# Kernel optimization log

Hardware: AMD Instinct MI355X
Metric: run time of the kernel (lower is better)

## Reference

```python
import jax, jax.numpy as jnp
import numpy as np

D_MODEL = 4096
N_Q_HEAD = 32
N_KV_HEAD = 8
HEAD_DIM = D_MODEL // N_Q_HEAD  # 128
N_REP = N_Q_HEAD // N_KV_HEAD   # 4
B, T = 2, 2048


def _rope_tables(seq_len, head_dim, dtype=jnp.float32):
    # theta_i = 10000^(-2*(i-1)/d) for i=1..d/2  (matches torch.pow(10000, -2*(arange(1,d/2+1)-1)/d))
    i = jnp.arange(head_dim // 2, dtype=dtype)
    theta = jnp.power(10000.0, -2.0 * i / head_dim)
    angles = jnp.outer(jnp.arange(seq_len, dtype=dtype), theta)  # [T, d/2]
    return jnp.cos(angles), jnp.sin(angles)


def _apply_rope(x, cos, sin):
    # x: [B, T, h, HD]; pairs are consecutive elements (view_as_complex semantics)
    B_, T_, h, hd = x.shape
    xp = x.reshape(B_, T_, h, hd // 2, 2)
    xr, xi = xp[..., 0], xp[..., 1]
    c = cos[None, :T_, None, :]
    s = sin[None, :T_, None, :]
    out_r = xr * c - xi * s
    out_i = xr * s + xi * c
    return jnp.stack([out_r, out_i], axis=-1).reshape(B_, T_, h, hd)


def setup_inputs() -> dict:
    key = jax.random.key(0)
    ks = jax.random.split(key, 5)
    scale = 0.02
    x = jax.random.normal(ks[0], (B, T, D_MODEL), dtype=jnp.float32)
    wq = jax.random.normal(ks[1], (D_MODEL, N_Q_HEAD * HEAD_DIM), dtype=jnp.float32) * scale
    wk = jax.random.normal(ks[2], (D_MODEL, N_KV_HEAD * HEAD_DIM), dtype=jnp.float32) * scale
    wv = jax.random.normal(ks[3], (D_MODEL, N_KV_HEAD * HEAD_DIM), dtype=jnp.float32) * scale
    wo = jax.random.normal(ks[4], (N_Q_HEAD * HEAD_DIM, D_MODEL), dtype=jnp.float32) * scale
    # causal mask: 1 where masked (strict upper triangle), per masked_fill(mask==1, -inf)
    attention_mask = jnp.triu(jnp.ones((T, T), dtype=jnp.int32), k=1)
    return {"x": x, "wq": wq, "wk": wk, "wv": wv, "wo": wo, "attention_mask": attention_mask}


def reference(x, wq, wk, wv, wo, attention_mask):
    B_, T_, _ = x.shape
    xq = (x @ wq).reshape(B_, T_, N_Q_HEAD, HEAD_DIM)
    xk = (x @ wk).reshape(B_, T_, N_KV_HEAD, HEAD_DIM)
    xv = (x @ wv).reshape(B_, T_, N_KV_HEAD, HEAD_DIM)

    cos, sin = _rope_tables(T_, HEAD_DIM, x.dtype)
    xq = _apply_rope(xq, cos, sin)
    xk = _apply_rope(xk, cos, sin)

    # GQA: repeat kv heads (training path: no cache)
    xk = jnp.repeat(xk, N_REP, axis=2)  # [B, T, HQ, HD]
    xv = jnp.repeat(xv, N_REP, axis=2)

    q = xq.transpose(0, 2, 1, 3)  # [B, H, T, HD]
    k = xk.transpose(0, 2, 1, 3)
    v = xv.transpose(0, 2, 1, 3)

    scores = jnp.einsum('bhqd,bhkd->bhqk', q, k) / jnp.sqrt(jnp.asarray(HEAD_DIM, x.dtype))
    scores = jnp.where(attention_mask[None, None, :, :] == 1, -jnp.inf, scores)
    probs = jax.nn.softmax(scores, axis=-1)
    out = jnp.einsum('bhqk,bhkd->bhqd', probs, v)
    out = out.transpose(0, 2, 1, 3).reshape(B_, T_, N_Q_HEAD * HEAD_DIM)
    return out @ wo
```

## Files before the change

kernel.cpp:

```cpp
#include <hip/hip_runtime.h>
#include <hip/hip_bf16.h>
#include <math.h>

typedef __hip_bfloat16 bf16;
typedef short bf16x8 __attribute__((ext_vector_type(8)));
typedef float f32x4 __attribute__((ext_vector_type(4)));
typedef float f32x16 __attribute__((ext_vector_type(16)));
typedef unsigned int u32;
typedef unsigned short u16;

#define GLD16(g, l)                                                            \
  __builtin_amdgcn_global_load_lds(                                            \
      (const __attribute__((address_space(1))) void*)(g),                      \
      (__attribute__((address_space(3))) void*)(l), 16, 0, 0)

#define SBAR() __builtin_amdgcn_s_barrier()
#define VMCNT(n) asm volatile("s_waitcnt vmcnt(" #n ")")
#define LGKM0() asm volatile("s_waitcnt lgkmcnt(0)")

__global__ void convert_f32_bf16(const float* __restrict__ in,
                                 bf16* __restrict__ out) {
  size_t i = ((size_t)blockIdx.x * 256 + threadIdx.x) * 4;
  float4 v = *(const float4*)(in + i);
  out[i + 0] = __float2bfloat16(v.x);
  out[i + 1] = __float2bfloat16(v.y);
  out[i + 2] = __float2bfloat16(v.z);
  out[i + 3] = __float2bfloat16(v.w);
}

__global__ void transpose_f32_bf16(const float* __restrict__ in,
                                   bf16* __restrict__ out, int R, int C) {
  __shared__ bf16 tile[32][33];
  int tx = threadIdx.x & 31, ty = threadIdx.x >> 5;
  int c0 = blockIdx.x * 32, r0 = blockIdx.y * 32;
#pragma unroll
  for (int i = 0; i < 32; i += 8)
    tile[ty + i][tx] = __float2bfloat16(in[(size_t)(r0 + ty + i) * C + c0 + tx]);
  __syncthreads();
#pragma unroll
  for (int i = 0; i < 32; i += 8)
    out[(size_t)(c0 + ty + i) * R + r0 + tx] = tile[tx][ty + i];
}

__global__ void transpose_v(const bf16* __restrict__ V, bf16* __restrict__ VT) {
  __shared__ bf16 tile[32][33];
  int s = blockIdx.z, b = s >> 3, kvh = s & 7;
  int t0 = blockIdx.x * 32, d0 = blockIdx.y * 32;
  int tx = threadIdx.x & 31, ty = threadIdx.x >> 5;
#pragma unroll
  for (int i = 0; i < 32; i += 8)
    tile[ty + i][tx] =
        V[(size_t)(b * 2048 + t0 + ty + i) * 6144 + kvh * 128 + d0 + tx];
  __syncthreads();
#pragma unroll
  for (int i = 0; i < 32; i += 8)
    VT[((size_t)s * 128 + d0 + ty + i) * 2048 + t0 + tx] = tile[tx][ty + i];
}

__global__ void rope_table_k(float* __restrict__ tab) {
  int idx = blockIdx.x * 256 + threadIdx.x;
  int t = idx >> 6, i = idx & 63;
  float theta = powf(10000.0f, -2.0f * (float)i / 128.0f);
  float ang = (float)t * theta;
  tab[idx * 2 + 0] = cosf(ang);
  tab[idx * 2 + 1] = sinf(ang);
}

__global__ void rope_apply(bf16* __restrict__ X, const float* __restrict__ tab,
                           int nheads, int rowstride, float omul) {
  size_t idx = (size_t)blockIdx.x * 256 + threadIdx.x;
  int i = (int)(idx & 63);
  size_t rest = idx >> 6;
  int h = (int)(rest % nheads);
  size_t r = rest / nheads;
  int t = (int)(r & 2047);
  float c = tab[(t * 64 + i) * 2 + 0];
  float s = tab[(t * 64 + i) * 2 + 1];
  bf16* p = X + r * (size_t)rowstride + h * 128 + 2 * i;
  float xr = __bfloat162float(p[0]), xi = __bfloat162float(p[1]);
  p[0] = __float2bfloat16((xr * c - xi * s) * omul);
  p[1] = __float2bfloat16((xr * s + xi * c) * omul);
}

template <typename OutT>
__global__ __launch_bounds__(512, 2) void gemm_bt8(const bf16* __restrict__ A,
                                                   const bf16* __restrict__ BT,
                                                   OutT* __restrict__ C, int M,
                                                   int N, int K) {
  __shared__ bf16 AS[2][2][128 * 64];
  __shared__ bf16 BS[2][2][128 * 64];

  const int tid = threadIdx.x;
  const int lane = tid & 63;
  const int w = tid >> 6, wm = w >> 2, wn = w & 3;
  const int lr = lane & 15, hi = lane >> 4;

  int gx = gridDim.x;
  int nwg = gx * gridDim.y;
  int bid = blockIdx.y * gx + blockIdx.x;
  int swz = (bid & 7) * (nwg >> 3) + (bid >> 3);
  const int m0 = (swz / gx) * 256, n0 = (swz % gx) * 256;

  const int NKT = K >> 6;
  const int NI = K >> 7;
  const int srow = tid >> 3;
  const int scol = ((tid & 7) ^ (srow & 7)) << 3;

  f32x4 acc[8][4];
#pragma unroll
  for (int m = 0; m < 8; ++m)
#pragma unroll
    for (int n = 0; n < 4; ++n)
#pragma unroll
      for (int j = 0; j < 4; ++j) acc[m][n][j] = 0.f;

  auto STAGE_A = [&](int buf, int kt) {
    int kk0 = (kt < NKT) ? kt * 64 : 0;
#pragma unroll
    for (int hs = 0; hs < 4; ++hs) {
      int ha = hs >> 1, sa = hs & 1;
      const bf16* g = A + (size_t)(m0 + ha * 128 + sa * 64 + srow) * K + kk0 + scol;
      GLD16(g, &AS[buf][ha][(sa * 64 + srow) * 64 + (tid & 7) * 8]);
    }
  };
  auto STAGE_B = [&](int buf, int kt, int half) {
    int kk0 = (kt < NKT) ? kt * 64 : 0;
#pragma unroll
    for (int sa = 0; sa < 2; ++sa) {
      const bf16* g =
          BT + (size_t)(n0 + half * 128 + sa * 64 + srow) * K + kk0 + scol;
      GLD16(g, &BS[buf][half][(sa * 64 + srow) * 64 + (tid & 7) * 8]);
    }
  };

  bf16x8 bfr[4][2], af[2][2];
  auto READ_B = [&](int buf) {
#pragma unroll
    for (int n = 0; n < 4; ++n) {
      int row = (wn & 1) * 64 + n * 16 + lr;
#pragma unroll
      for (int kk = 0; kk < 2; ++kk)
        bfr[n][kk] = *(const bf16x8*)(&BS[buf][wn >> 1]
                                         [row * 64 + (((kk * 4 + hi) ^ (row & 7)) << 3)]);
    }
  };
  auto READ_A = [&](int buf, int q) {
#pragma unroll
    for (int mm = 0; mm < 2; ++mm) {
      int row = (q * 2 + mm) * 16 + lr;
#pragma unroll
      for (int kk = 0; kk < 2; ++kk)
        af[mm][kk] = *(const bf16x8*)(&AS[buf][wm]
                                         [row * 64 + (((kk * 4 + hi) ^ (row & 7)) << 3)]);
    }
  };

#define MFMA16(q)                                                              \
  do {                                                                         \
    LGKM0();                                                                   \
    __builtin_amdgcn_s_setprio(1);                                             \
    _Pragma("unroll") for (int mm = 0; mm < 2; ++mm)                           \
        _Pragma("unroll") for (int n = 0; n < 4; ++n)                          \
        _Pragma("unroll") for (int kk = 0; kk < 2; ++kk)                       \
            acc[(q) * 2 + mm][n] = __builtin_amdgcn_mfma_f32_16x16x32_bf16(    \
                af[mm][kk], bfr[n][kk], acc[(q) * 2 + mm][n], 0, 0, 0);        \
    __builtin_amdgcn_s_setprio(0);                                             \
  } while (0)

  STAGE_A(0, 0);
  STAGE_B(0, 0, 0);
  STAGE_B(0, 0, 1);
  STAGE_B(1, 1, 0);
  STAGE_B(1, 1, 1);
  VMCNT(4);
  SBAR();

  for (int i = 0; i < NI; ++i) {
    int t = 2 * i;
    READ_B(0); READ_A(0, 0); STAGE_A(1, t + 1);
    SBAR(); MFMA16(0); SBAR();
    READ_A(0, 1); STAGE_B(0, t + 2, 0);
    SBAR(); MFMA16(1); SBAR();
    READ_A(0, 2); STAGE_B(0, t + 2, 1);
    SBAR(); MFMA16(2); SBAR();
    READ_A(0, 3);
    SBAR(); MFMA16(3); VMCNT(4); SBAR();
    READ_B(1); READ_A(1, 0); STAGE_A(0, t + 2);
    SBAR(); MFMA16(0); SBAR();
    READ_A(1, 1); STAGE_B(1, t + 3, 0);
    SBAR(); MFMA16(1); SBAR();
    READ_A(1, 2); STAGE_B(1, t + 3, 1);
    SBAR(); MFMA16(2); SBAR();
    READ_A(1, 3);
    SBAR(); MFMA16(3); VMCNT(4); SBAR();
  }

  VMCNT(0);
  SBAR();

#pragma unroll
  for (int m = 0; m < 8; ++m) {
    int row_base = m0 + wm * 128 + m * 16 + hi * 4;
#pragma unroll
    for (int n = 0; n < 4; ++n) {
      int col = n0 + wn * 64 + n * 16 + lr;
#pragma unroll
      for (int j = 0; j < 4; ++j) {
        float v = acc[m][n][j];
        if constexpr (sizeof(OutT) == 2)
          C[(size_t)(row_base + j) * N + col] = (OutT)__float2bfloat16(v);
        else
          C[(size_t)(row_base + j) * N + col] = (OutT)v;
      }
    }
  }
#undef MFMA16
}

static __device__ inline u32 cvtpk_bf16(float a, float b) {
  u32 r;
  asm("v_cvt_pk_bf16_f32 %0, %1, %2" : "=v"(r) : "v"(a), "v"(b));
  return r;
}

__global__ __launch_bounds__(512) void flash_attn3(const bf16* __restrict__ Q,
                                                   const bf16* __restrict__ K,
                                                   const bf16* __restrict__ VT,
                                                   bf16* __restrict__ AO) {
  __shared__ bf16 Kbuf[2][64 * 128];
  __shared__ bf16 Vbuf[2][128 * 64];

  int bid = blockIdx.x;
  int b = bid >> 8;
  int i = (bid >> 3) & 31;
  int kvh = bid & 7;
  int hq = i >> 3;
  int qt = 7 - (i & 7);
  int h = kvh * 4 + hq;

  const int tid = threadIdx.x;
  const int lane = tid & 63, w = tid >> 6;
  const int ql = lane & 31, hi = lane >> 5;
  const int qrow0 = qt * 256 + w * 32;
  const int nt = 4 * qt + 4;

  const bf16* Kg0 = K + (size_t)b * 2048 * 6144 + kvh * 128;
  const bf16* Vg0 = VT + (size_t)(b * 8 + kvh) * 128 * 2048;

  bf16x8 qf[8];
  {
    const bf16* qb =
        Q + (size_t)(b * 2048 + qrow0 + ql) * 6144 + h * 128 + hi * 8;
#pragma unroll
    for (int dc = 0; dc < 8; ++dc) qf[dc] = *(const bf16x8*)(qb + dc * 16);
  }

  f32x16 O[4];
#pragma unroll
  for (int d4 = 0; d4 < 4; ++d4)
#pragma unroll
    for (int e = 0; e < 16; ++e) O[d4][e] = 0.f;
  float m_ = -1e30f, l_ = 0.f;

  auto STAGE = [&](int buf, int kv0) {
    bf16* Ks = &Kbuf[buf][0];
    bf16* Vs = &Vbuf[buf][0];
    const bf16* Kg = Kg0 + (size_t)kv0 * 6144;
    const bf16* Vg = Vg0 + kv0;
#pragma unroll
    for (int it = 0; it < 2; ++it) {
      int s = it * 512 + tid;
      int row = s >> 4, c = s & 15;
      GLD16(Kg + (size_t)row * 6144 + ((c ^ (row & 7)) << 3), Ks + s * 8);
    }
#pragma unroll
    for (int it = 0; it < 2; ++it) {
      int s = it * 512 + tid;
      int row = s >> 3, c = s & 7;
      GLD16(Vg + (size_t)row * 2048 + ((c ^ (row & 7)) << 3), Vs + s * 8);
    }
  };

  STAGE(0, 0);
  __syncthreads();

  for (int t = 0; t < nt; ++t) {
    int kv0 = t * 64;
    if (t + 1 < nt) STAGE((t + 1) & 1, kv0 + 64);

    if (kv0 <= qrow0 + 31) {
      const bf16* Ks = &Kbuf[t & 1][0];
      const bf16* Vs = &Vbuf[t & 1][0];

      f32x16 Sx[2];
#pragma unroll
      for (int cb = 0; cb < 2; ++cb)
#pragma unroll
        for (int e = 0; e < 16; ++e) Sx[cb][e] = 0.f;

      __builtin_amdgcn_s_setprio(1);
#pragma unroll
      for (int cb = 0; cb < 2; ++cb) {
        int krow = cb * 32 + ql;
#pragma unroll
        for (int dc = 0; dc < 8; ++dc) {
          bf16x8 kf = *(const bf16x8*)(Ks + krow * 128 +
                                       (((dc * 2 + hi) ^ (ql & 7)) << 3));
          Sx[cb] = __builtin_amdgcn_mfma_f32_32x32x16_bf16(kf, qf[dc], Sx[cb],
                                                           0, 0, 0);
        }
      }
      __builtin_amdgcn_s_setprio(0);

      int q = qrow0 + ql;
      bool domask = (kv0 + 63 > qrow0);
      if (domask) {
#pragma unroll
        for (int cb = 0; cb < 2; ++cb)
#pragma unroll
          for (int r = 0; r < 16; ++r) {
            int kv = kv0 + cb * 32 + (r & 3) + 8 * (r >> 2) + 4 * hi;
            if (kv > q) Sx[cb][r] = -1e30f;
          }
      }
      float pm = -1e30f;
#pragma unroll
      for (int cb = 0; cb < 2; ++cb)
#pragma unroll
        for (int r = 0; r < 16; ++r) pm = fmaxf(pm, Sx[cb][r]);
      pm = fmaxf(pm, __shfl_xor(pm, 32));

      if (!__all(pm - m_ <= 11.5416f)) {
        float nm = fmaxf(m_, pm);
        float rs = exp2f(m_ - nm);
        m_ = nm;
        l_ *= rs;
#pragma unroll
        for (int d4 = 0; d4 < 4; ++d4)
#pragma unroll
          for (int e = 0; e < 16; ++e) O[d4][e] *= rs;
      }
      float ps = 0.f;
#pragma unroll
      for (int cb = 0; cb < 2; ++cb)
#pragma unroll
        for (int r = 0; r < 16; ++r) {
          float p = exp2f(Sx[cb][r] - m_);
          Sx[cb][r] = p;
          ps += p;
        }
      ps += __shfl_xor(ps, 32);
      l_ += ps;

      bf16x8 pb[4];
#pragma unroll
      for (int kb = 0; kb < 4; ++kb) {
        int cb = kb >> 1, r0 = 8 * (kb & 1);
        u32 Av = cvtpk_bf16(Sx[cb][r0 + 0], Sx[cb][r0 + 1]);
        u32 Bv = cvtpk_bf16(Sx[cb][r0 + 2], Sx[cb][r0 + 3]);
        u32 Cv = cvtpk_bf16(Sx[cb][r0 + 4], Sx[cb][r0 + 5]);
        u32 Dv = cvtpk_bf16(Sx[cb][r0 + 6], Sx[cb][r0 + 7]);
        u32 sA = (u32)__shfl_xor((int)Av, 32);
        u32 sB = (u32)__shfl_xor((int)Bv, 32);
        u32 sC = (u32)__shfl_xor((int)Cv, 32);
        u32 sD = (u32)__shfl_xor((int)Dv, 32);
        union { u32 u[4]; bf16x8 v; } pk;
        pk.u[0] = hi ? sC : Av;
        pk.u[1] = hi ? sD : Bv;
        pk.u[2] = hi ? Cv : sA;
        pk.u[3] = hi ? Dv : sB;
        pb[kb] = pk.v;
      }

      __builtin_amdgcn_s_setprio(1);
#pragma unroll
      for (int d4 = 0; d4 < 4; ++d4) {
        int vrow = d4 * 32 + ql;
#pragma unroll
        for (int kb = 0; kb < 4; ++kb) {
          bf16x8 vf = *(const bf16x8*)(Vs + vrow * 64 +
                                       (((kb * 2 + hi) ^ (ql & 7)) << 3));
          O[d4] = __builtin_amdgcn_mfma_f32_32x32x16_bf16(vf, pb[kb], O[d4], 0,
                                                          0, 0);
        }
      }
      __builtin_amdgcn_s_setprio(0);
    }
    __syncthreads();
  }

  float inv = 1.0f / l_;
  bf16* outp = AO + (size_t)(b * 2048 + qrow0 + ql) * 4096 + h * 128;
#pragma unroll
  for (int d4 = 0; d4 < 4; ++d4)
#pragma unroll
    for (int rg = 0; rg < 4; ++rg) {
      union { u16 s[4]; unsigned long long v; } pk;
#pragma unroll
      for (int j = 0; j < 4; ++j)
        pk.s[j] = __bfloat16_as_ushort(__float2bfloat16(O[d4][rg * 4 + j] * inv));
      *(unsigned long long*)(outp + d4 * 32 + rg * 8 + hi * 4) = pk.v;
    }
}

extern "C" void kernel_launch(void* const* d_in, const int* in_sizes, int n_in,
                              void* d_out, int out_size, void* d_ws,
                              size_t ws_size, hipStream_t stream) {
  const float* x = (const float*)d_in[0];
  const float* wq = (const float*)d_in[1];
  const float* wk = (const float*)d_in[2];
  const float* wv = (const float*)d_in[3];
  const float* wo = (const float*)d_in[4];

  char* ws = (char*)d_ws;
  bf16* xb    = (bf16*)(ws + 0);
  bf16* WqkvT = (bf16*)(ws + 33554432);
  bf16* WoT   = (bf16*)(ws + 83886080);
  bf16* QKV   = (bf16*)(ws + 117440512);
  bf16* VTb   = (bf16*)(ws + 167772160);
  float* tab  = (float*)(ws + 176160768);
  bf16* AOb   = xb;

  const float LOG2E = 1.4426950408889634f;
  const float ISQ = 0.08838834764831845f;

  convert_f32_bf16<<<16384, 256, 0, stream>>>(x, xb);
  transpose_f32_bf16<<<dim3(128, 128), 256, 0, stream>>>(wq, WqkvT, 4096, 4096);
  transpose_f32_bf16<<<dim3(32, 128), 256, 0, stream>>>(
      wk, WqkvT + (size_t)4096 * 4096, 4096, 1024);
  transpose_f32_bf16<<<dim3(32, 128), 256, 0, stream>>>(
      wv, WqkvT + (size_t)5120 * 4096, 4096, 1024);
  transpose_f32_bf16<<<dim3(128, 128), 256, 0, stream>>>(wo, WoT, 4096, 4096);
  rope_table_k<<<512, 256, 0, stream>>>(tab);

  gemm_bt8<bf16><<<dim3(24, 16), 512, 0, stream>>>(xb, WqkvT, QKV, 4096, 6144,
                                                   4096);

  rope_apply<<<32768, 256, 0, stream>>>(QKV, tab, 32, 6144, LOG2E * ISQ);
  rope_apply<<<8192, 256, 0, stream>>>(QKV + 4096, tab, 8, 6144, 1.0f);

  transpose_v<<<dim3(64, 4, 16), 256, 0, stream>>>(QKV + 5120, VTb);

  flash_attn3<<<512, 512, 0, stream>>>(QKV, QKV + 4096, VTb, AOb);

  gemm_bt8<float><<<dim3(16, 16), 512, 0, stream>>>(AOb, WoT, (float*)d_out,
                                                    4096, 4096, 4096);
}
```

Measured before the change: 619.5 us.

## Double-buffer LDS fragment registers to overlap reads with MFMA in GEMM loop

New measurement: 640.0 us. 1.03x slower.

```diff
diff --git a/kernel.cpp b/kernel.cpp
--- a/kernel.cpp
+++ b/kernel.cpp
@@ -16,7 +16,6 @@
 
 #define SBAR() __builtin_amdgcn_s_barrier()
 #define VMCNT(n) asm volatile("s_waitcnt vmcnt(" #n ")")
-#define LGKM0() asm volatile("s_waitcnt lgkmcnt(0)")
 
 __global__ void convert_f32_bf16(const float* __restrict__ in,
                                  bf16* __restrict__ out) {
@@ -133,37 +132,38 @@
     }
   };
 
-  bf16x8 bfr[4][2], af[2][2];
-  auto READ_B = [&](int buf) {
+  bf16x8 B0[4][2], B1[4][2];
+  bf16x8 af0[2][2], af1[2][2];
+
+  auto READ_B_TO = [&](bf16x8(&dst)[4][2], int buf) {
 #pragma unroll
     for (int n = 0; n < 4; ++n) {
       int row = (wn & 1) * 64 + n * 16 + lr;
 #pragma unroll
       for (int kk = 0; kk < 2; ++kk)
-        bfr[n][kk] = *(const bf16x8*)(&BS[buf][wn >> 1]
+        dst[n][kk] = *(const bf16x8*)(&BS[buf][wn >> 1]
                                          [row * 64 + (((kk * 4 + hi) ^ (row & 7)) << 3)]);
     }
   };
-  auto READ_A = [&](int buf, int q) {
+  auto READ_A_TO = [&](bf16x8(&dst)[2][2], int buf, int q) {
 #pragma unroll
     for (int mm = 0; mm < 2; ++mm) {
       int row = (q * 2 + mm) * 16 + lr;
 #pragma unroll
       for (int kk = 0; kk < 2; ++kk)
-        af[mm][kk] = *(const bf16x8*)(&AS[buf][wm]
-                                         [row * 64 + (((kk * 4 + hi) ^ (row & 7)) << 3)]);
+        dst[mm][kk] = *(const bf16x8*)(&AS[buf][wm]
+                                          [row * 64 + (((kk * 4 + hi) ^ (row & 7)) << 3)]);
     }
   };
 
-#define MFMA16(q)                                                              \
+#define MFMA16(q, AF, BR)                                                      \
   do {                                                                         \
-    LGKM0();                                                                   \
     __builtin_amdgcn_s_setprio(1);                                             \
     _Pragma("unroll") for (int mm = 0; mm < 2; ++mm)                           \
         _Pragma("unroll") for (int n = 0; n < 4; ++n)                          \
         _Pragma("unroll") for (int kk = 0; kk < 2; ++kk)                       \
             acc[(q) * 2 + mm][n] = __builtin_amdgcn_mfma_f32_16x16x32_bf16(    \
-                af[mm][kk], bfr[n][kk], acc[(q) * 2 + mm][n], 0, 0, 0);        \
+                AF[mm][kk], BR[n][kk], acc[(q) * 2 + mm][n], 0, 0, 0);         \
     __builtin_amdgcn_s_setprio(0);                                             \
   } while (0)
 
@@ -174,25 +174,27 @@
   STAGE_B(1, 1, 1);
   VMCNT(4);
   SBAR();
+  READ_B_TO(B0, 0);
+  READ_A_TO(af0, 0, 0);
 
   for (int i = 0; i < NI; ++i) {
     int t = 2 * i;
-    READ_B(0); READ_A(0, 0); STAGE_A(1, t + 1);
-    SBAR(); MFMA16(0); SBAR();
-    READ_A(0, 1); STAGE_B(0, t + 2, 0);
-    SBAR(); MFMA16(1); SBAR();
-    READ_A(0, 2); STAGE_B(0, t + 2, 1);
-    SBAR(); MFMA16(2); SBAR();
-    READ_A(0, 3);
-    SBAR(); MFMA16(3); VMCNT(4); SBAR();
-    READ_B(1); READ_A(1, 0); STAGE_A(0, t + 2);
-    SBAR(); MFMA16(0); SBAR();
-    READ_A(1, 1); STAGE_B(1, t + 3, 0);
-    SBAR(); MFMA16(1); SBAR();
-    READ_A(1, 2); STAGE_B(1, t + 3, 1);
-    SBAR(); MFMA16(2); SBAR();
-    READ_A(1, 3);
-    SBAR(); MFMA16(3); VMCNT(4); SBAR();
+    READ_A_TO(af1, 0, 1); STAGE_A(1, t + 1);
+    SBAR(); MFMA16(0, af0, B0); SBAR();
+    READ_A_TO(af0, 0, 2); STAGE_B(0, t + 2, 0);
+    SBAR(); MFMA16(1, af1, B0); SBAR();
+    READ_A_TO(af1, 0, 3); STAGE_B(0, t + 2, 1);
+    SBAR(); MFMA16(2, af0, B0); VMCNT(4); SBAR();
+    READ_B_TO(B1, 1); READ_A_TO(af0, 1, 0);
+    SBAR(); MFMA16(3, af1, B0); SBAR();
+    READ_A_TO(af1, 1, 1); STAGE_A(0, t + 2);
+    SBAR(); MFMA16(0, af0, B1); SBAR();
+    READ_A_TO(af0, 1, 2); STAGE_B(1, t + 3, 0);
+    SBAR(); MFMA16(1, af1, B1); SBAR();
+    READ_A_TO(af1, 1, 3); STAGE_B(1, t + 3, 1);
+    SBAR(); MFMA16(2, af0, B1); VMCNT(4); SBAR();
+    READ_B_TO(B0, 0); READ_A_TO(af0, 0, 0);
+    SBAR(); MFMA16(3, af1, B1); SBAR();
   }
 
   VMCNT(0);
```
